# Optimization experiments

Hardware: AMD Instinct MI355X
Metric: run time of the kernel (lower is better)

Reference implementation:

```python
import jax, jax.numpy as jnp
import numpy as np

XL, YL, XH, YH = 0.0, 0.0, 1000.0, 1000.0
NUM_MOVABLE = 1_000_000
NUM_FILLER = 200_000
NUM_NODES = NUM_MOVABLE + NUM_FILLER  # movable first, filler last (no fixed nodes)
RB_X = RB_Y = 512
PB_X = PB_Y = 512
MAX_ROUTE_RATE = 2.0
MIN_ROUTE_RATE = 1.0 / MAX_ROUTE_RATE
ROUTE_EXP = 2.5
MAX_PIN_RATE = 2.5
MIN_PIN_RATE = 1.0 / MAX_PIN_RATE
TOTAL_PLACE_AREA = 1.0e6
TOTAL_WHITESPACE = 5.0e5
AREA_STOP = 0.01
ROUTE_STOP = 0.01
PIN_STOP = 0.05
K = 3  # max bins a node can overlap per axis (node size < 2 * bin size)


def _bin_overlap_area(px, py, sx, sy, util, bsx, bsy, nbx, nby):
    """Per-node sum over overlapped bins of overlap_area * utilization.
    Faithful to adjust_node_area kernel: area_i = sum_b ovl_x * ovl_y * util[b]."""
    x_hi = px + sx
    y_hi = py + sy
    bx0 = jnp.floor((px - XL) / bsx).astype(jnp.int32)
    by0 = jnp.floor((py - YL) / bsy).astype(jnp.int32)
    ks = jnp.arange(K, dtype=jnp.int32)
    bx = bx0[:, None] + ks          # [N, K]
    by = by0[:, None] + ks
    bxc = jnp.clip(bx, 0, nbx - 1)
    byc = jnp.clip(by, 0, nby - 1)
    blx = XL + bxc.astype(util.dtype) * bsx
    bly = YL + byc.astype(util.dtype) * bsy
    ox = jnp.maximum(jnp.minimum(x_hi[:, None], blx + bsx) - jnp.maximum(px[:, None], blx), 0.0)
    oy = jnp.maximum(jnp.minimum(y_hi[:, None], bly + bsy) - jnp.maximum(py[:, None], bly), 0.0)
    ox = jnp.where((bx >= 0) & (bx < nbx), ox, 0.0)  # kill clipped duplicates
    oy = jnp.where((by >= 0) & (by < nby), oy, 0.0)
    u = util[bxc[:, :, None], byc[:, None, :]]       # [N, K, K] gather
    return jnp.einsum('nk,nl,nkl->n', ox, oy, u)


def setup_inputs() -> dict:
    key = jax.random.key(0)
    k1, k2, k3, k4, k5, k6, k7 = jax.random.split(key, 7)
    # sizes in [0.2, 1.2] (< bin size 1.953 -> each node spans <= 2 bins/axis)
    node_size_x = 0.2 + jax.random.uniform(k1, (NUM_NODES,), jnp.float32)
    node_size_y = 0.2 + jax.random.uniform(k2, (NUM_NODES,), jnp.float32)
    pos_x = jax.random.uniform(k3, (NUM_NODES,), jnp.float32) * (XH - 1.5)
    pos_y = jax.random.uniform(k4, (NUM_NODES,), jnp.float32) * (YH - 1.5)
    pos = jnp.concatenate([pos_x, pos_y])
    route_utilization_map = 0.5 + 1.3 * jax.random.uniform(k5, (RB_X, RB_Y), jnp.float32)
    pin_utilization_map = 0.3 + 1.7 * jax.random.uniform(k6, (PB_X, PB_Y), jnp.float32)
    pin_offset_x = jax.random.normal(k7, (1024,), jnp.float32)
    pin_offset_y = jax.random.normal(jax.random.fold_in(k7, 1), (1024,), jnp.float32)
    target_density = jnp.ones((1,), jnp.float32)
    return {
        'pos': pos,
        'node_size_x': node_size_x,
        'node_size_y': node_size_y,
        'pin_offset_x': pin_offset_x,
        'pin_offset_y': pin_offset_y,
        'target_density': target_density,
        'route_utilization_map': route_utilization_map,
        'pin_utilization_map': pin_utilization_map,
    }


def reference(pos, node_size_x, node_size_y, pin_offset_x, pin_offset_y,
              target_density, route_utilization_map, pin_utilization_map):
    num_nodes = NUM_NODES
    bsx_r = (XH - XL) / RB_X
    bsy_r = (YH - YL) / RB_Y
    bsx_p = (XH - XL) / PB_X
    bsy_p = (YH - YL) / PB_Y

    nsx_m = node_size_x[:NUM_MOVABLE]
    nsy_m = node_size_y[:NUM_MOVABLE]
    px_m = pos[:NUM_MOVABLE]
    py_m = pos[num_nodes:num_nodes + NUM_MOVABLE]
    old_area = nsx_m * nsy_m
    old_sum = old_area.sum()

    nsx_f = node_size_x[-NUM_FILLER:]
    nsy_f = node_size_y[-NUM_FILLER:]
    px_f = pos[num_nodes - NUM_FILLER:num_nodes]
    py_f = pos[2 * num_nodes - NUM_FILLER:]
    old_filler_sum = (nsx_f * nsy_f).sum()

    route_clamped = jnp.clip(route_utilization_map ** ROUTE_EXP, MIN_ROUTE_RATE, MAX_ROUTE_RATE)
    route_opt_area = _bin_overlap_area(px_m, py_m, nsx_m, nsy_m, route_clamped, bsx_r, bsy_r, RB_X, RB_Y)
    pin_clamped = jnp.clip(pin_utilization_map, MIN_PIN_RATE, MAX_PIN_RATE)
    pin_opt_area = _bin_overlap_area(px_m, py_m, nsx_m, nsy_m, pin_clamped, bsx_p, bsy_p, PB_X, PB_Y)

    area_increment = jax.nn.relu(jnp.maximum(route_opt_area, pin_opt_area) - old_area)
    inc_sum = area_increment.sum()
    budget = jnp.minimum(0.1 * TOTAL_WHITESPACE, TOTAL_PLACE_AREA - old_sum)
    raw_scale = budget / inc_sum
    scale = jnp.clip(raw_scale, 0.0, 1.0)
    new_area = jnp.where(raw_scale <= 0.0, old_area, old_area + area_increment * scale)
    inc_sum_eff = jnp.where(raw_scale <= 0.0, 0.0, inc_sum * scale)
    new_sum = old_sum + inc_sum_eff
    area_ratio = inc_sum_eff / old_sum

    route_flag = (jax.nn.relu(route_opt_area - old_area).sum() / old_sum) > ROUTE_STOP
    pin_flag = (jax.nn.relu(pin_opt_area - old_area).sum() / old_sum) > PIN_STOP
    adjust = (area_ratio > AREA_STOP) & (route_flag | pin_flag)

    # movable inflation, keeping node centers fixed
    mratio = jnp.sqrt(new_area / old_area)
    new_nsx_m = jnp.where(adjust, nsx_m * mratio, nsx_m)
    new_nsy_m = jnp.where(adjust, nsy_m * mratio, nsy_m)
    new_px_m = jnp.where(adjust, px_m + 0.5 * (nsx_m - new_nsx_m), px_m)
    new_py_m = jnp.where(adjust, py_m + 0.5 * (nsy_m - new_nsy_m), py_m)

    # filler shrink if total area overflows
    fcond = adjust & ((new_sum + old_filler_sum) > TOTAL_PLACE_AREA)
    fratio = jnp.sqrt(jax.nn.relu(TOTAL_PLACE_AREA - new_sum) / old_filler_sum)
    new_nsx_f = jnp.where(fcond, nsx_f * fratio, nsx_f)
    new_nsy_f = jnp.where(fcond, nsy_f * fratio, nsy_f)
    new_px_f = jnp.where(fcond, px_f + 0.5 * (nsx_f - new_nsx_f), px_f)
    new_py_f = jnp.where(fcond, py_f + 0.5 * (nsy_f - new_nsy_f), py_f)

    new_pos = jnp.concatenate([new_px_m, new_px_f, new_py_m, new_py_f])
    new_nsx = jnp.concatenate([new_nsx_m, new_nsx_f])
    new_nsy = jnp.concatenate([new_nsy_m, new_nsy_f])
    return (new_pos, new_nsx, new_nsy)
```

## Files before the change

kernel.cpp:

```cpp
#include <hip/hip_runtime.h>
#include <hip/hip_fp16.h>
#include <math.h>

#define NUM_MOVABLE 1000000
#define NUM_FILLER  200000
#define NUM_NODES   1200000
#define NBX 512
#define NBY 512
#define THREADS 256
#define NGROUPS 300000
#define MGROUPS 250000
#define PREP_BLOCKS 1024
#define P1_BLOCKS ((MGROUPS + THREADS - 1) / THREADS)
#define AP_BLOCKS ((NGROUPS + THREADS - 1) / THREADS)

static constexpr float BSX = 1000.0f / 512.0f;
static constexpr float TOTAL_PLACE_AREA = 1000000.0f;
static constexpr float TOTAL_WHITESPACE = 500000.0f;
static constexpr float AREA_STOP  = 0.01f;
static constexpr float ROUTE_STOP = 0.01f;
static constexpr float PIN_STOP   = 0.05f;

struct alignas(16) Quad { __half2 r0; __half2 r1; __half2 p0; __half2 p1; };

__device__ __forceinline__ float route_val(const float* m, int idx) {
    return fminf(fmaxf(powf(m[idx], 2.5f), 0.5f), 2.0f);
}
__device__ __forceinline__ float pin_val(const float* m, int idx) {
    return fminf(fmaxf(m[idx], 0.4f), 2.5f);
}

__global__ void prep_kernel(const float* __restrict__ route,
                            const float* __restrict__ pin,
                            const float* __restrict__ nsx,
                            const float* __restrict__ nsy,
                            Quad* __restrict__ qmap,
                            float* __restrict__ pf) {
    int i = blockIdx.x * THREADS + threadIdx.x;
    {
        int bx = i >> 9, by = i & 511;
        int bx1 = min(bx + 1, NBX - 1), by1 = min(by + 1, NBY - 1);
        int i00 = bx * NBY + by,  i01 = bx * NBY + by1;
        int i10 = bx1 * NBY + by, i11 = bx1 * NBY + by1;
        Quad q;
        q.r0 = __halves2half2(__float2half(route_val(route, i00)),
                              __float2half(route_val(route, i01)));
        q.r1 = __halves2half2(__float2half(route_val(route, i10)),
                              __float2half(route_val(route, i11)));
        q.p0 = __halves2half2(__float2half(pin_val(pin, i00)),
                              __float2half(pin_val(pin, i01)));
        q.p1 = __halves2half2(__float2half(pin_val(pin, i10)),
                              __float2half(pin_val(pin, i11)));
        qmap[i] = q;
    }
    float s = 0.f;
    if (i < NUM_FILLER) {
        int j = NUM_MOVABLE + i;
        s = nsx[j] * nsy[j];
    }
    __shared__ float red[4];
    #pragma unroll
    for (int o = 32; o >= 1; o >>= 1) s += __shfl_down(s, o, 64);
    int wid = threadIdx.x >> 6, lid = threadIdx.x & 63;
    if (lid == 0) red[wid] = s;
    __syncthreads();
    if (threadIdx.x == 0)
        pf[blockIdx.x] = red[0] + red[1] + red[2] + red[3];
}

__global__ void pass1_kernel(const float* __restrict__ pos,
                             const float* __restrict__ nsx,
                             const float* __restrict__ nsy,
                             const Quad* __restrict__ qmap,
                             float* __restrict__ inc,
                             float4* __restrict__ part4) {
    int t = blockIdx.x * THREADS + threadIdx.x;
    float s_old = 0.f, s_inc = 0.f, s_r = 0.f, s_p = 0.f;

    if (t < MGROUPS) {
        float4 px4 = ((const float4*)pos)[t];
        float4 py4 = ((const float4*)(pos + NUM_NODES))[t];
        float4 sx4 = ((const float4*)nsx)[t];
        float4 sy4 = ((const float4*)nsy)[t];

        Quad q[4];
        float wx0[4], wx1[4], wy0[4], wy1[4];
        #pragma unroll
        for (int j = 0; j < 4; ++j) {
            float px = (&px4.x)[j], py = (&py4.x)[j];
            float sx = (&sx4.x)[j], sy = (&sy4.x)[j];
            float hix = px + sx, hiy = py + sy;
            int b0x = (int)floorf(px / BSX);
            int b0y = (int)floorf(py / BSX);
            float ex = (float)(b0x + 1) * BSX;
            float ey = (float)(b0y + 1) * BSX;
            wx0[j] = fminf(hix, ex) - px;
            wx1[j] = fmaxf(hix - ex, 0.0f);
            wy0[j] = fminf(hiy, ey) - py;
            wy1[j] = fmaxf(hiy - ey, 0.0f);
            q[j] = qmap[b0x * NBY + b0y];
        }
        float ai4[4];
        #pragma unroll
        for (int j = 0; j < 4; ++j) {
            float2 r0 = __half22float2(q[j].r0), r1 = __half22float2(q[j].r1);
            float2 p0 = __half22float2(q[j].p0), p1 = __half22float2(q[j].p1);
            float r = wx0[j] * (wy0[j] * r0.x + wy1[j] * r0.y)
                    + wx1[j] * (wy0[j] * r1.x + wy1[j] * r1.y);
            float p = wx0[j] * (wy0[j] * p0.x + wy1[j] * p0.y)
                    + wx1[j] * (wy0[j] * p1.x + wy1[j] * p1.y);
            float sx = (&sx4.x)[j], sy = (&sy4.x)[j];
            float old_a = sx * sy;
            float ai = fmaxf(fmaxf(r, p) - old_a, 0.0f);
            ai4[j] = ai;
            s_old += old_a;
            s_inc += ai;
            s_r += fmaxf(r - old_a, 0.0f);
            s_p += fmaxf(p - old_a, 0.0f);
        }
        ((float4*)inc)[t] = make_float4(ai4[0], ai4[1], ai4[2], ai4[3]);
    }

    __shared__ float red[4][4];
    #pragma unroll
    for (int o = 32; o >= 1; o >>= 1) {
        s_old += __shfl_down(s_old, o, 64);
        s_inc += __shfl_down(s_inc, o, 64);
        s_r   += __shfl_down(s_r, o, 64);
        s_p   += __shfl_down(s_p, o, 64);
    }
    int wid = threadIdx.x >> 6, lid = threadIdx.x & 63;
    if (lid == 0) { red[wid][0] = s_old; red[wid][1] = s_inc;
                    red[wid][2] = s_r;   red[wid][3] = s_p; }
    __syncthreads();
    if (threadIdx.x == 0) {
        float a0 = 0.f, a1 = 0.f, a2 = 0.f, a3 = 0.f;
        for (int w = 0; w < 4; ++w) {
            a0 += red[w][0]; a1 += red[w][1]; a2 += red[w][2]; a3 += red[w][3];
        }
        part4[blockIdx.x] = make_float4(a0, a1, a2, a3);
    }
}

__global__ void apply_kernel(const float* __restrict__ pos,
                             const float* __restrict__ nsx,
                             const float* __restrict__ nsy,
                             const float* __restrict__ inc,
                             const float4* __restrict__ part4,
                             const float* __restrict__ pf,
                             float* __restrict__ out) {
    __shared__ float red[4][5];
    __shared__ float der[4];
    {
        float t0 = 0.f, t1 = 0.f, t2 = 0.f, t3 = 0.f, t4 = 0.f;
        for (int b = threadIdx.x; b < P1_BLOCKS; b += THREADS) {
            float4 v = part4[b];
            t0 += v.x; t1 += v.y; t2 += v.z; t3 += v.w;
        }
        for (int b = threadIdx.x; b < PREP_BLOCKS; b += THREADS) t4 += pf[b];
        #pragma unroll
        for (int o = 32; o >= 1; o >>= 1) {
            t0 += __shfl_down(t0, o, 64);
            t1 += __shfl_down(t1, o, 64);
            t2 += __shfl_down(t2, o, 64);
            t3 += __shfl_down(t3, o, 64);
            t4 += __shfl_down(t4, o, 64);
        }
        int wid = threadIdx.x >> 6, lid = threadIdx.x & 63;
        if (lid == 0) { red[wid][0] = t0; red[wid][1] = t1; red[wid][2] = t2;
                        red[wid][3] = t3; red[wid][4] = t4; }
        __syncthreads();
        if (threadIdx.x == 0) {
            float old_sum = 0.f, inc_sum = 0.f, route_ex = 0.f, pin_ex = 0.f, filler_sum = 0.f;
            for (int w = 0; w < 4; ++w) {
                old_sum += red[w][0]; inc_sum += red[w][1]; route_ex += red[w][2];
                pin_ex += red[w][3]; filler_sum += red[w][4];
            }
            float budget = fminf(0.1f * TOTAL_WHITESPACE, TOTAL_PLACE_AREA - old_sum);
            float raw = budget / inc_sum;
            float scale = fminf(fmaxf(raw, 0.0f), 1.0f);
            float scale_eff = (raw <= 0.0f) ? 0.0f : scale;
            float inc_eff = (raw <= 0.0f) ? 0.0f : inc_sum * scale;
            float new_sum = old_sum + inc_eff;
            float area_ratio = inc_eff / old_sum;
            bool route_flag = (route_ex / old_sum) > ROUTE_STOP;
            bool pin_flag = (pin_ex / old_sum) > PIN_STOP;
            bool adjust = (area_ratio > AREA_STOP) && (route_flag || pin_flag);
            bool fcond = adjust && (new_sum + filler_sum > TOTAL_PLACE_AREA);
            float fratio = sqrtf(fmaxf(TOTAL_PLACE_AREA - new_sum, 0.0f) / filler_sum);
            der[0] = adjust ? 1.0f : 0.0f;
            der[1] = scale_eff;
            der[2] = fcond ? 1.0f : 0.0f;
            der[3] = fratio;
        }
        __syncthreads();
    }
    const float adjust = der[0], scale_eff = der[1];
    const float fcond = der[2], fratio = der[3];

    int t = blockIdx.x * THREADS + threadIdx.x;
    if (t >= NGROUPS) return;

    float4 px4 = ((const float4*)pos)[t];
    float4 py4 = ((const float4*)(pos + NUM_NODES))[t];
    float4 sx4 = ((const float4*)nsx)[t];
    float4 sy4 = ((const float4*)nsy)[t];
    float nx[4], ny[4], opx[4], opy[4];

    if (t < MGROUPS) {
        float4 ai4 = ((const float4*)inc)[t];
        #pragma unroll
        for (int j = 0; j < 4; ++j) {
            float px = (&px4.x)[j], py = (&py4.x)[j];
            float sx = (&sx4.x)[j], sy = (&sy4.x)[j];
            nx[j] = sx; ny[j] = sy; opx[j] = px; opy[j] = py;
            if (adjust > 0.5f) {
                float old_a = sx * sy;
                float na = old_a + (&ai4.x)[j] * scale_eff;
                float mr = sqrtf(na / old_a);
                nx[j] = sx * mr; ny[j] = sy * mr;
                opx[j] = px + 0.5f * (sx - nx[j]);
                opy[j] = py + 0.5f * (sy - ny[j]);
            }
        }
    } else {
        #pragma unroll
        for (int j = 0; j < 4; ++j) {
            float px = (&px4.x)[j], py = (&py4.x)[j];
            float sx = (&sx4.x)[j], sy = (&sy4.x)[j];
            nx[j] = sx; ny[j] = sy; opx[j] = px; opy[j] = py;
            if (fcond > 0.5f) {
                nx[j] = sx * fratio; ny[j] = sy * fratio;
                opx[j] = px + 0.5f * (sx - nx[j]);
                opy[j] = py + 0.5f * (sy - ny[j]);
            }
        }
    }
    ((float4*)out)[t]                   = make_float4(opx[0], opx[1], opx[2], opx[3]);
    ((float4*)(out + NUM_NODES))[t]     = make_float4(opy[0], opy[1], opy[2], opy[3]);
    ((float4*)(out + 2 * NUM_NODES))[t] = make_float4(nx[0], nx[1], nx[2], nx[3]);
    ((float4*)(out + 3 * NUM_NODES))[t] = make_float4(ny[0], ny[1], ny[2], ny[3]);
}

extern "C" void kernel_launch(void* const* d_in, const int* in_sizes, int n_in,
                              void* d_out, int out_size, void* d_ws, size_t ws_size,
                              hipStream_t stream) {
    const float* pos       = (const float*)d_in[0];
    const float* node_sx   = (const float*)d_in[1];
    const float* node_sy   = (const float*)d_in[2];
    const float* route_map = (const float*)d_in[6];
    const float* pin_map   = (const float*)d_in[7];
    float* out = (float*)d_out;

    char*   ws    = (char*)d_ws;
    Quad*   qmap  = (Quad*)ws;
    float*  inc   = (float*)(ws + sizeof(Quad) * NBX * NBY);
    float4* part4 = (float4*)((char*)inc + sizeof(float) * NUM_MOVABLE);
    float*  pf    = (float*)(part4 + P1_BLOCKS);

    hipLaunchKernelGGL(prep_kernel, dim3(PREP_BLOCKS), dim3(THREADS), 0, stream,
                       route_map, pin_map, node_sx, node_sy, qmap, pf);
    hipLaunchKernelGGL(pass1_kernel, dim3(P1_BLOCKS), dim3(THREADS), 0, stream,
                       pos, node_sx, node_sy, qmap, inc, part4);
    hipLaunchKernelGGL(apply_kernel, dim3(AP_BLOCKS), dim3(THREADS), 0, stream,
                       pos, node_sx, node_sy, inc, part4, pf, out);
}
```

Baseline: 107.3 us.

## Move filler-area reduction into pass1, prefetch apply inputs, use nontemporal stores

The filler-area reduction moves out of the map-prep kernel into pass1, whose grid now also covers the filler groups. Each pass1 block writes a per-block filler partial alongside the other partial sums. The apply kernel issues its per-node loads before the global reduction and barrier, so memory latency overlaps the scalar decision step. Output writes use nontemporal stores to avoid polluting cache. In exchange, the reduction loop in apply reads slightly more partials, and idle threads load a clamped index.

```diff
diff --git a/kernel.cpp b/kernel.cpp
--- a/kernel.cpp
+++ b/kernel.cpp
@@ -11,7 +11,7 @@
 #define NGROUPS 300000
 #define MGROUPS 250000
 #define PREP_BLOCKS 1024
-#define P1_BLOCKS ((MGROUPS + THREADS - 1) / THREADS)
+#define P1_BLOCKS ((NGROUPS + THREADS - 1) / THREADS)
 #define AP_BLOCKS ((NGROUPS + THREADS - 1) / THREADS)
 
 static constexpr float BSX = 1000.0f / 512.0f;
@@ -21,6 +21,8 @@
 static constexpr float ROUTE_STOP = 0.01f;
 static constexpr float PIN_STOP   = 0.05f;
 
+typedef float vfloat4 __attribute__((ext_vector_type(4)));
+
 struct alignas(16) Quad { __half2 r0; __half2 r1; __half2 p0; __half2 p1; };
 
 __device__ __forceinline__ float route_val(const float* m, int idx) {
@@ -32,40 +34,22 @@
 
 __global__ void prep_kernel(const float* __restrict__ route,
                             const float* __restrict__ pin,
-                            const float* __restrict__ nsx,
-                            const float* __restrict__ nsy,
-                            Quad* __restrict__ qmap,
-                            float* __restrict__ pf) {
+                            Quad* __restrict__ qmap) {
     int i = blockIdx.x * THREADS + threadIdx.x;
-    {
-        int bx = i >> 9, by = i & 511;
-        int bx1 = min(bx + 1, NBX - 1), by1 = min(by + 1, NBY - 1);
-        int i00 = bx * NBY + by,  i01 = bx * NBY + by1;
-        int i10 = bx1 * NBY + by, i11 = bx1 * NBY + by1;
-        Quad q;
-        q.r0 = __halves2half2(__float2half(route_val(route, i00)),
-                              __float2half(route_val(route, i01)));
-        q.r1 = __halves2half2(__float2half(route_val(route, i10)),
-                              __float2half(route_val(route, i11)));
-        q.p0 = __halves2half2(__float2half(pin_val(pin, i00)),
-                              __float2half(pin_val(pin, i01)));
-        q.p1 = __halves2half2(__float2half(pin_val(pin, i10)),
-                              __float2half(pin_val(pin, i11)));
-        qmap[i] = q;
-    }
-    float s = 0.f;
-    if (i < NUM_FILLER) {
-        int j = NUM_MOVABLE + i;
-        s = nsx[j] * nsy[j];
-    }
-    __shared__ float red[4];
-    #pragma unroll
-    for (int o = 32; o >= 1; o >>= 1) s += __shfl_down(s, o, 64);
-    int wid = threadIdx.x >> 6, lid = threadIdx.x & 63;
-    if (lid == 0) red[wid] = s;
-    __syncthreads();
-    if (threadIdx.x == 0)
-        pf[blockIdx.x] = red[0] + red[1] + red[2] + red[3];
+    int bx = i >> 9, by = i & 511;
+    int bx1 = min(bx + 1, NBX - 1), by1 = min(by + 1, NBY - 1);
+    int i00 = bx * NBY + by,  i01 = bx * NBY + by1;
+    int i10 = bx1 * NBY + by, i11 = bx1 * NBY + by1;
+    Quad q;
+    q.r0 = __halves2half2(__float2half(route_val(route, i00)),
+                          __float2half(route_val(route, i01)));
+    q.r1 = __halves2half2(__float2half(route_val(route, i10)),
+                          __float2half(route_val(route, i11)));
+    q.p0 = __halves2half2(__float2half(pin_val(pin, i00)),
+                          __float2half(pin_val(pin, i01)));
+    q.p1 = __halves2half2(__float2half(pin_val(pin, i10)),
+                          __float2half(pin_val(pin, i11)));
+    qmap[i] = q;
 }
 
 __global__ void pass1_kernel(const float* __restrict__ pos,
@@ -73,9 +57,10 @@
                              const float* __restrict__ nsy,
                              const Quad* __restrict__ qmap,
                              float* __restrict__ inc,
-                             float4* __restrict__ part4) {
+                             float4* __restrict__ part4,
+                             float* __restrict__ pf) {
     int t = blockIdx.x * THREADS + threadIdx.x;
-    float s_old = 0.f, s_inc = 0.f, s_r = 0.f, s_p = 0.f;
+    float s_old = 0.f, s_inc = 0.f, s_r = 0.f, s_p = 0.f, sf = 0.f;
 
     if (t < MGROUPS) {
         float4 px4 = ((const float4*)pos)[t];
@@ -119,26 +104,33 @@
             s_p += fmaxf(p - old_a, 0.0f);
         }
         ((float4*)inc)[t] = make_float4(ai4[0], ai4[1], ai4[2], ai4[3]);
-    }
-
-    __shared__ float red[4][4];
+    } else if (t < NGROUPS) {
+        float4 sx4 = ((const float4*)nsx)[t];
+        float4 sy4 = ((const float4*)nsy)[t];
+        sf = sx4.x * sy4.x + sx4.y * sy4.y + sx4.z * sy4.z + sx4.w * sy4.w;
+    }
+
+    __shared__ float red[4][5];
     #pragma unroll
     for (int o = 32; o >= 1; o >>= 1) {
         s_old += __shfl_down(s_old, o, 64);
         s_inc += __shfl_down(s_inc, o, 64);
         s_r   += __shfl_down(s_r, o, 64);
         s_p   += __shfl_down(s_p, o, 64);
+        sf    += __shfl_down(sf, o, 64);
     }
     int wid = threadIdx.x >> 6, lid = threadIdx.x & 63;
     if (lid == 0) { red[wid][0] = s_old; red[wid][1] = s_inc;
-                    red[wid][2] = s_r;   red[wid][3] = s_p; }
+                    red[wid][2] = s_r;   red[wid][3] = s_p; red[wid][4] = sf; }
     __syncthreads();
     if (threadIdx.x == 0) {
-        float a0 = 0.f, a1 = 0.f, a2 = 0.f, a3 = 0.f;
+        float a0 = 0.f, a1 = 0.f, a2 = 0.f, a3 = 0.f, a4 = 0.f;
         for (int w = 0; w < 4; ++w) {
-            a0 += red[w][0]; a1 += red[w][1]; a2 += red[w][2]; a3 += red[w][3];
+            a0 += red[w][0]; a1 += red[w][1]; a2 += red[w][2];
+            a3 += red[w][3]; a4 += red[w][4];
         }
         part4[blockIdx.x] = make_float4(a0, a1, a2, a3);
+        pf[blockIdx.x] = a4;
     }
 }
 
@@ -149,6 +141,16 @@
                              const float4* __restrict__ part4,
                              const float* __restrict__ pf,
                              float* __restrict__ out) {
+    int t = blockIdx.x * THREADS + threadIdx.x;
+    bool active = t < NGROUPS;
+    int tc = active ? t : 0;
+
+    float4 px4 = ((const float4*)pos)[tc];
+    float4 py4 = ((const float4*)(pos + NUM_NODES))[tc];
+    float4 sx4 = ((const float4*)nsx)[tc];
+    float4 sy4 = ((const float4*)nsy)[tc];
+    float4 ai4 = ((const float4*)inc)[tc < MGROUPS ? tc : 0];
+
     __shared__ float red[4][5];
     __shared__ float der[4];
     {
@@ -156,8 +158,8 @@
         for (int b = threadIdx.x; b < P1_BLOCKS; b += THREADS) {
             float4 v = part4[b];
             t0 += v.x; t1 += v.y; t2 += v.z; t3 += v.w;
-        }
-        for (int b = threadIdx.x; b < PREP_BLOCKS; b += THREADS) t4 += pf[b];
+            t4 += pf[b];
+        }
         #pragma unroll
         for (int o = 32; o >= 1; o >>= 1) {
             t0 += __shfl_down(t0, o, 64);
@@ -195,20 +197,12 @@
         }
         __syncthreads();
     }
+    if (!active) return;
     const float adjust = der[0], scale_eff = der[1];
     const float fcond = der[2], fratio = der[3];
 
-    int t = blockIdx.x * THREADS + threadIdx.x;
-    if (t >= NGROUPS) return;
-
-    float4 px4 = ((const float4*)pos)[t];
-    float4 py4 = ((const float4*)(pos + NUM_NODES))[t];
-    float4 sx4 = ((const float4*)nsx)[t];
-    float4 sy4 = ((const float4*)nsy)[t];
     float nx[4], ny[4], opx[4], opy[4];
-
     if (t < MGROUPS) {
-        float4 ai4 = ((const float4*)inc)[t];
         #pragma unroll
         for (int j = 0; j < 4; ++j) {
             float px = (&px4.x)[j], py = (&py4.x)[j];
@@ -236,10 +230,14 @@
             }
         }
     }
-    ((float4*)out)[t]                   = make_float4(opx[0], opx[1], opx[2], opx[3]);
-    ((float4*)(out + NUM_NODES))[t]     = make_float4(opy[0], opy[1], opy[2], opy[3]);
-    ((float4*)(out + 2 * NUM_NODES))[t] = make_float4(nx[0], nx[1], nx[2], nx[3]);
-    ((float4*)(out + 3 * NUM_NODES))[t] = make_float4(ny[0], ny[1], ny[2], ny[3]);
+    vfloat4 vx = {opx[0], opx[1], opx[2], opx[3]};
+    vfloat4 vy = {opy[0], opy[1], opy[2], opy[3]};
+    vfloat4 vnx = {nx[0], nx[1], nx[2], nx[3]};
+    vfloat4 vny = {ny[0], ny[1], ny[2], ny[3]};
+    __builtin_nontemporal_store(vx,  (vfloat4*)out + t);
+    __builtin_nontemporal_store(vy,  (vfloat4*)(out + NUM_NODES) + t);
+    __builtin_nontemporal_store(vnx, (vfloat4*)(out + 2 * NUM_NODES) + t);
+    __builtin_nontemporal_store(vny, (vfloat4*)(out + 3 * NUM_NODES) + t);
 }
 
 extern "C" void kernel_launch(void* const* d_in, const int* in_sizes, int n_in,
@@ -259,9 +257,9 @@
     float*  pf    = (float*)(part4 + P1_BLOCKS);
 
     hipLaunchKernelGGL(prep_kernel, dim3(PREP_BLOCKS), dim3(THREADS), 0, stream,
-                       route_map, pin_map, node_sx, node_sy, qmap, pf);
+                       route_map, pin_map, qmap);
     hipLaunchKernelGGL(pass1_kernel, dim3(P1_BLOCKS), dim3(THREADS), 0, stream,
-                       pos, node_sx, node_sy, qmap, inc, part4);
+                       pos, node_sx, node_sy, qmap, inc, part4, pf);
     hipLaunchKernelGGL(apply_kernel, dim3(AP_BLOCKS), dim3(THREADS), 0, stream,
                        pos, node_sx, node_sy, inc, part4, pf, out);
 }
```

Result: no change. 107.3 us (+0.1%).
